# Performance work log

Hardware: AMD Instinct MI355X
Metric: run time of the kernel (lower is better)

## Reference

```python
import jax, jax.numpy as jnp
import numpy as np

N_NODES = 100000

def _norm_coeffs(edge_index, n_nodes):
    # PyG GCNConv default: add self-loops, symmetric normalization D^-1/2 A D^-1/2
    src = jnp.concatenate([edge_index[0], jnp.arange(n_nodes, dtype=edge_index.dtype)])
    dst = jnp.concatenate([edge_index[1], jnp.arange(n_nodes, dtype=edge_index.dtype)])
    deg = jax.ops.segment_sum(jnp.ones_like(dst, dtype=jnp.float32), dst, num_segments=n_nodes)
    dinv = jnp.where(deg > 0, jax.lax.rsqrt(deg), 0.0)
    norm = dinv[src] * dinv[dst]  # [E + N]
    return src, dst, norm

def _gcn_conv(x, W, b, src, dst, norm, n_nodes):
    h = x @ W                       # [N, out] dense transform first (PyG order)
    msg = h[src] * norm[:, None]    # gather + scale, [E+N, out]
    out = jax.ops.segment_sum(msg, dst, num_segments=n_nodes)  # scatter-add aggregate
    return out + b

def setup_inputs() -> dict:
    key = jax.random.key(0)
    ks = jax.random.split(key, 8)
    in_feats, h_feats, num_classes = 128, 128, 64
    n_edges = 1_600_000
    x = jax.random.normal(ks[0], (N_NODES, in_feats), dtype=jnp.float32)
    edge_index = jax.random.randint(ks[1], (2, n_edges), 0, N_NODES, dtype=jnp.int64)
    def glorot(k, fi, fo):
        s = jnp.sqrt(6.0 / (fi + fo))
        return jax.random.uniform(k, (fi, fo), jnp.float32, -s, s)
    return {
        "x": x,
        "edge_index": edge_index,
        "W0": glorot(ks[2], in_feats, h_feats), "b0": jnp.zeros((h_feats,), jnp.float32),
        "W1": glorot(ks[3], h_feats, h_feats), "b1": jnp.zeros((h_feats,), jnp.float32),
        "W2": glorot(ks[4], h_feats, num_classes), "b2": jnp.zeros((num_classes,), jnp.float32),
    }

def reference(x, edge_index, W0, b0, W1, b1, W2, b2):
    n_nodes = x.shape[0]
    src, dst, norm = _norm_coeffs(edge_index, n_nodes)
    # layer 0 + 1: ReLU between (dropout is identity in eval mode)
    h = jax.nn.relu(_gcn_conv(x, W0, b0, src, dst, norm, n_nodes))
    h = jax.nn.relu(_gcn_conv(h, W1, b1, src, dst, norm, n_nodes))
    # final layer: no activation
    return _gcn_conv(h, W2, b2, src, dst, norm, n_nodes)
```

## Files before the change

kernel.cpp:

```cpp
#include <hip/hip_runtime.h>
#include <hip/hip_bf16.h>
#include <stdint.h>


typedef __attribute__((ext_vector_type(8))) short bf16x8;
typedef __attribute__((ext_vector_type(4))) float f32x4;

__device__ __forceinline__ float bflo(uint32_t u) { return __uint_as_float(u << 16); }
__device__ __forceinline__ float bfhi(uint32_t u) { return __uint_as_float(u & 0xffff0000u); }
__device__ __forceinline__ unsigned short f2bf(float f) {
    uint32_t x = __float_as_uint(f);
    return (unsigned short)((x + 0x7fffu + ((x >> 16) & 1u)) >> 16);
}

__global__ __launch_bounds__(256) void k_deg_rank(const int* __restrict__ dst,
                                                  int* __restrict__ deg,
                                                  int* __restrict__ rank, int E) {
    int e = blockIdx.x * 256 + threadIdx.x;
    if (e < E) rank[e] = atomicAdd(&deg[dst[e]], 1);
}

__global__ __launch_bounds__(256) void k_dinv(const int* __restrict__ deg,
                                              float* __restrict__ dinv, int N) {
    int i = blockIdx.x * 256 + threadIdx.x;
    if (i < N) dinv[i] = rsqrtf((float)(deg[i] + 1));
}

__global__ __launch_bounds__(256) void k_scan_local(const int* __restrict__ deg,
                                                    int* __restrict__ incl,
                                                    int* __restrict__ bsum, int N) {
    __shared__ int part[256];
    int t = threadIdx.x;
    int idx0 = blockIdx.x * 1024 + t * 4;
    int4 lv = {0, 0, 0, 0};
    if (idx0 + 4 <= N) {
        lv = *(const int4*)&deg[idx0];
    } else {
        int* pv = (int*)&lv;
        for (int i = 0; i < 4; ++i) pv[i] = (idx0 + i < N) ? deg[idx0 + i] : 0;
    }
    int s = lv.x + lv.y + lv.z + lv.w;
    part[t] = s;
    __syncthreads();
    for (int off = 1; off < 256; off <<= 1) {
        int x = (t >= off) ? part[t - off] : 0;
        __syncthreads();
        part[t] += x;
        __syncthreads();
    }
    int run = (t == 0) ? 0 : part[t - 1];
    if (t == 255) bsum[blockIdx.x] = part[255];
    int4 ov;
    ov.x = run + lv.x;
    ov.y = ov.x + lv.y;
    ov.z = ov.y + lv.z;
    ov.w = ov.z + lv.w;
    if (idx0 + 4 <= N) {
        *(int4*)&incl[idx0] = ov;
    } else {
        int* po = (int*)&ov;
        for (int i = 0; i < 4; ++i)
            if (idx0 + i < N) incl[idx0 + i] = po[i];
    }
}

__global__ __launch_bounds__(256) void k_scan_tops(int* __restrict__ bsum, int nb,
                                                   int* __restrict__ row_ptr, int N) {
    __shared__ int part[256];
    int t = threadIdx.x;
    int v = (t < nb) ? bsum[t] : 0;
    part[t] = v;
    __syncthreads();
    for (int off = 1; off < 256; off <<= 1) {
        int x = (t >= off) ? part[t - off] : 0;
        __syncthreads();
        part[t] += x;
        __syncthreads();
    }
    if (t < nb) bsum[t] = part[t] - v;
    if (t == 255) row_ptr[N] = part[255];
}

__global__ __launch_bounds__(256) void k_scan_final(const int* __restrict__ incl,
                                                    const int* __restrict__ deg,
                                                    const int* __restrict__ bsum,
                                                    int* __restrict__ row_ptr, int N) {
    int i = blockIdx.x * 256 + threadIdx.x;
    if (i < N) row_ptr[i] = incl[i] - deg[i] + bsum[i >> 10];
}

__global__ __launch_bounds__(256) void k_scatter(const int* __restrict__ src,
                                                 const int* __restrict__ dst,
                                                 const int* __restrict__ rank,
                                                 const int* __restrict__ row_ptr,
                                                 int* __restrict__ col_idx, int E) {
    int e = blockIdx.x * 256 + threadIdx.x;
    if (e < E) {
        int d = dst[e];
        col_idx[row_ptr[d] + rank[e]] = src[e];
    }
}

__global__ __launch_bounds__(256) void k_prepw(const float* __restrict__ W0,
                                               const float* __restrict__ W1,
                                               const float* __restrict__ W2,
                                               unsigned short* __restrict__ wt0,
                                               unsigned short* __restrict__ wt1,
                                               unsigned short* __restrict__ wt2) {
    int id = blockIdx.x * 256 + threadIdx.x;
    const float* Wsrc;
    unsigned short* dst;
    int t, M, plane;
    if (id < 16384)      { t = id;         Wsrc = W0; dst = wt0; M = 128; plane = 16384; }
    else if (id < 32768) { t = id - 16384; Wsrc = W1; dst = wt1; M = 128; plane = 16384; }
    else if (id < 40960) { t = id - 32768; Wsrc = W2; dst = wt2; M = 64;  plane = 8192;  }
    else return;
    int k = (M == 128) ? (t >> 7) : (t >> 6);
    int c = (M == 128) ? (t & 127) : (t & 63);
    float v = Wsrc[k * M + c];
    unsigned short hi = f2bf(v);
    float lov = v - bflo((uint32_t)hi);
    dst[c * 128 + k]         = hi;
    dst[plane + c * 128 + k] = f2bf(lov);
}

template <int NCOL>
__global__ __launch_bounds__(256) void k_gemm_mfma(
    const float* __restrict__ A, const unsigned short* __restrict__ Wt,
    const float* __restrict__ dinv, unsigned short* __restrict__ H, int N) {
    constexpr int K = 128, KT = 64;
    constexpr int A_PLANE = 128 * KT;
    constexpr int W_PLANE = NCOL * KT;
    __shared__ __align__(16) unsigned short sm[2 * A_PLANE + 2 * W_PLANE];
    unsigned short* Ah  = sm;
    unsigned short* Al  = sm + A_PLANE;
    unsigned short* Whp = sm + 2 * A_PLANE;
    unsigned short* Wlp = sm + 2 * A_PLANE + W_PLANE;

    const int tid = threadIdx.x;
    const long r0 = (long)blockIdx.x * 128;
    const int w = tid >> 6, l = tid & 63;
    const int lr = l & 15, lk = l >> 4;
    constexpr int WR = (NCOL == 128) ? 4 : 2;
    const int wrow = (NCOL == 128) ? (w >> 1) * 64 : w * 32;
    const int wcol = (NCOL == 128) ? (w & 1) * 64 : 0;

    f32x4 acc[WR][4];
#pragma unroll
    for (int i = 0; i < WR; ++i)
#pragma unroll
        for (int j = 0; j < 4; ++j) acc[i][j] = (f32x4){0.f, 0.f, 0.f, 0.f};

    for (int kt = 0; kt < 2; ++kt) {
        if (kt) __syncthreads();
#pragma unroll
        for (int it = 0; it < 4; ++it) {
            int id = it * 256 + tid;
            int r = id >> 3, kc = id & 7;
            long gr = r0 + r;
            if (gr >= N) gr = N - 1;
            const float* ap = &A[gr * K + kt * KT + kc * 8];
            float4 v0 = *(const float4*)ap;
            float4 v1 = *(const float4*)(ap + 4);
            float vv[8] = {v0.x, v0.y, v0.z, v0.w, v1.x, v1.y, v1.z, v1.w};
            union { unsigned short u[8]; bf16x8 v; } ph, pl;
#pragma unroll
            for (int j = 0; j < 8; ++j) {
                unsigned short h = f2bf(vv[j]);
                ph.u[j] = h;
                pl.u[j] = f2bf(vv[j] - bflo((uint32_t)h));
            }
            int boff = r * 128 + ((kc * 16) ^ ((r & 7) << 4));
            *(bf16x8*)((char*)Ah + boff) = ph.v;
            *(bf16x8*)((char*)Al + boff) = pl.v;
        }
#pragma unroll
        for (int it = 0; it < NCOL / 32; ++it) {
            int id = it * 256 + tid;
            int c = id >> 3, kc = id & 7;
            const unsigned short* wp = &Wt[c * K + kt * KT + kc * 8];
            bf16x8 vh = *(const bf16x8*)wp;
            bf16x8 vl = *(const bf16x8*)(wp + NCOL * K);
            int boff = c * 128 + ((kc * 16) ^ ((c & 7) << 4));
            *(bf16x8*)((char*)Whp + boff) = vh;
            *(bf16x8*)((char*)Wlp + boff) = vl;
        }
        __syncthreads();
#pragma unroll
        for (int ks = 0; ks < 2; ++ks) {
            int kb = ks * 64 + lk * 16;
            bf16x8 bh[4], bl[4];
#pragma unroll
            for (int cf = 0; cf < 4; ++cf) {
                int c = wcol + cf * 16 + lr;
                int off = c * 128 + (kb ^ ((c & 7) << 4));
                bh[cf] = *(bf16x8*)((char*)Whp + off);
                bl[cf] = *(bf16x8*)((char*)Wlp + off);
            }
#pragma unroll
            for (int rf = 0; rf < WR; ++rf) {
                int r = wrow + rf * 16 + lr;
                int off = r * 128 + (kb ^ ((r & 7) << 4));
                bf16x8 ah = *(bf16x8*)((char*)Ah + off);
                bf16x8 al = *(bf16x8*)((char*)Al + off);
#pragma unroll
                for (int cf = 0; cf < 4; ++cf) {
                    acc[rf][cf] = __builtin_amdgcn_mfma_f32_16x16x32_bf16(ah, bh[cf], acc[rf][cf], 0, 0, 0);
                    acc[rf][cf] = __builtin_amdgcn_mfma_f32_16x16x32_bf16(al, bh[cf], acc[rf][cf], 0, 0, 0);
                    acc[rf][cf] = __builtin_amdgcn_mfma_f32_16x16x32_bf16(ah, bl[cf], acc[rf][cf], 0, 0, 0);
                }
            }
        }
    }
#pragma unroll
    for (int rf = 0; rf < WR; ++rf) {
        long rb = r0 + wrow + rf * 16 + lk * 4;
#pragma unroll
        for (int reg = 0; reg < 4; ++reg) {
            long r = rb + reg;
            if (r < N) {
                float dv = dinv[r];
#pragma unroll
                for (int cf = 0; cf < 4; ++cf) {
                    int c = wcol + cf * 16 + lr;
                    H[r * NCOL + c] = f2bf(dv * acc[rf][cf][reg]);
                }
            }
        }
    }
}

template <int F, bool RELU>
__global__ __launch_bounds__(256) void k_agg(const unsigned short* __restrict__ H,
                                             const int* __restrict__ row_ptr,
                                             const int* __restrict__ col_idx,
                                             const float* __restrict__ dinv,
                                             const float* __restrict__ bias,
                                             float* __restrict__ Y, int N) {
    int lane = threadIdx.x & 63;
    int node = blockIdx.x * 4 + (threadIdx.x >> 6);
    if (node >= N) return;

    float acc0, acc1 = 0.f;
    if constexpr (F == 128) {
        uint32_t u = *(const uint32_t*)&H[(size_t)node * 128 + lane * 2];
        acc0 = bflo(u);
        acc1 = bfhi(u);
    } else {
        acc0 = bflo((uint32_t)H[(size_t)node * F + lane]);
    }

    int start = row_ptr[node], end = row_ptr[node + 1];
    for (int base = start; base < end; base += 64) {
        int n = end - base;
        int sidx = 0;
        if (lane < n) sidx = col_idx[base + lane];
        int cnt = n < 64 ? n : 64;
        int j = 0;
        for (; j + 4 <= cnt; j += 4) {
            int s0 = __shfl(sidx, j),     s1 = __shfl(sidx, j + 1);
            int s2 = __shfl(sidx, j + 2), s3 = __shfl(sidx, j + 3);
            if constexpr (F == 128) {
                uint32_t u0 = *(const uint32_t*)&H[(size_t)s0 * 128 + lane * 2];
                uint32_t u1 = *(const uint32_t*)&H[(size_t)s1 * 128 + lane * 2];
                uint32_t u2 = *(const uint32_t*)&H[(size_t)s2 * 128 + lane * 2];
                uint32_t u3 = *(const uint32_t*)&H[(size_t)s3 * 128 + lane * 2];
                acc0 += bflo(u0); acc1 += bfhi(u0);
                acc0 += bflo(u1); acc1 += bfhi(u1);
                acc0 += bflo(u2); acc1 += bfhi(u2);
                acc0 += bflo(u3); acc1 += bfhi(u3);
            } else {
                acc0 += bflo((uint32_t)H[(size_t)s0 * F + lane]);
                acc0 += bflo((uint32_t)H[(size_t)s1 * F + lane]);
                acc0 += bflo((uint32_t)H[(size_t)s2 * F + lane]);
                acc0 += bflo((uint32_t)H[(size_t)s3 * F + lane]);
            }
        }
        for (; j < cnt; ++j) {
            int s = __shfl(sidx, j);
            if constexpr (F == 128) {
                uint32_t u = *(const uint32_t*)&H[(size_t)s * 128 + lane * 2];
                acc0 += bflo(u);
                acc1 += bfhi(u);
            } else {
                acc0 += bflo((uint32_t)H[(size_t)s * F + lane]);
            }
        }
    }

    float dv = dinv[node];
    if constexpr (F == 128) {
        float2 b = *(const float2*)&bias[lane * 2];
        float y0 = dv * acc0 + b.x, y1 = dv * acc1 + b.y;
        if (RELU) { y0 = fmaxf(y0, 0.f); y1 = fmaxf(y1, 0.f); }
        float2 o; o.x = y0; o.y = y1;
        *(float2*)&Y[(size_t)node * 128 + lane * 2] = o;
    } else {
        float y = dv * acc0 + bias[lane];
        if (RELU) y = fmaxf(y, 0.f);
        Y[(size_t)node * F + lane] = y;
    }
}

extern "C" void kernel_launch(void* const* d_in, const int* in_sizes, int n_in,
                              void* d_out, int out_size, void* d_ws, size_t ws_size,
                              hipStream_t stream) {
    const float* x  = (const float*)d_in[0];
    const int* eidx = (const int*)d_in[1];
    const float* W0 = (const float*)d_in[2];
    const float* b0 = (const float*)d_in[3];
    const float* W1 = (const float*)d_in[4];
    const float* b1 = (const float*)d_in[5];
    const float* W2 = (const float*)d_in[6];
    const float* b2 = (const float*)d_in[7];
    float* out = (float*)d_out;

    const int N = in_sizes[0] / 128;
    const int E = in_sizes[1] / 2;
    const int* srcp = eidx;
    const int* dstp = eidx + E;

    char* p = (char*)d_ws;
    auto take = [&](size_t bytes) {
        char* r = p;
        p += (bytes + 255) & ~(size_t)255;
        return r;
    };
    int*            deg     = (int*)take((size_t)N * 4);
    int*            rank    = (int*)take((size_t)E * 4);
    int*            row_ptr = (int*)take((size_t)(N + 1) * 4);
    float*          dinv    = (float*)take((size_t)N * 4);
    int*            col_idx = (int*)take((size_t)E * 4);
    unsigned short* hbuf    = (unsigned short*)take((size_t)N * 128 * 2);
    float*          ybuf    = (float*)take((size_t)N * 128 * 4);
    int*            incl    = (int*)take((size_t)N * 4);
    int*            bsum    = (int*)take((size_t)256 * 4);
    unsigned short* wt0     = (unsigned short*)take((size_t)2 * 16384 * 2);
    unsigned short* wt1     = (unsigned short*)take((size_t)2 * 16384 * 2);
    unsigned short* wt2     = (unsigned short*)take((size_t)2 * 8192 * 2);

    hipMemsetAsync(deg, 0, (size_t)N * 4, stream);

    k_deg_rank<<<(E + 255) / 256, 256, 0, stream>>>(dstp, deg, rank, E);
    k_dinv<<<(N + 255) / 256, 256, 0, stream>>>(deg, dinv, N);
    k_prepw<<<160, 256, 0, stream>>>(W0, W1, W2, wt0, wt1, wt2);

    int nb = (N + 1023) / 1024;
    k_scan_local<<<nb, 256, 0, stream>>>(deg, incl, bsum, N);
    k_scan_tops<<<1, 256, 0, stream>>>(bsum, nb, row_ptr, N);
    k_scan_final<<<(N + 255) / 256, 256, 0, stream>>>(incl, deg, bsum, row_ptr, N);

    k_scatter<<<(E + 255) / 256, 256, 0, stream>>>(srcp, dstp, rank, row_ptr,
                                                   col_idx, E);

    int gemm_grid = (N + 127) / 128;
    int agg_grid  = (N + 3) / 4;

    k_gemm_mfma<128><<<gemm_grid, 256, 0, stream>>>(x, wt0, dinv, hbuf, N);
    k_agg<128, true><<<agg_grid, 256, 0, stream>>>(hbuf, row_ptr, col_idx,
                                                   dinv, b0, ybuf, N);
    k_gemm_mfma<128><<<gemm_grid, 256, 0, stream>>>(ybuf, wt1, dinv, hbuf, N);
    k_agg<128, true><<<agg_grid, 256, 0, stream>>>(hbuf, row_ptr, col_idx,
                                                   dinv, b1, ybuf, N);
    k_gemm_mfma<64><<<gemm_grid, 256, 0, stream>>>(ybuf, wt2, dinv, hbuf, N);
    k_agg<64, false><<<agg_grid, 256, 0, stream>>>(hbuf, row_ptr, col_idx,
                                                   dinv, b2, out, N);
}
```

Measured before the change: 457.3 us.

## Privatize degree-count atomics per XCC to cut cross-die contention

The degree histogram and rank atomics are split into eight per-XCC count arrays, indexed by the hardware XCC id, so atomics from different dies hit different cache lines. A merge kernel turns the per-XCC counts into exclusive offsets and computes the total degree and dinv. The scatter then adds the XCC offset to the local rank. This costs an 8x larger memset and counter buffer plus an extra read in the scatter, in exchange for more local atomics.

Result: no change. 462.6 us (+1.2%).

```diff
diff --git a/kernel.cpp b/kernel.cpp
--- a/kernel.cpp
+++ b/kernel.cpp
@@ -13,17 +13,38 @@
     return (unsigned short)((x + 0x7fffu + ((x >> 16) & 1u)) >> 16);
 }
 
+__device__ __forceinline__ int xcc_id() {
+    int x;
+    asm volatile("s_getreg_b32 %0, hwreg(HW_REG_XCC_ID)" : "=s"(x));
+    return x & 7;
+}
+
 __global__ __launch_bounds__(256) void k_deg_rank(const int* __restrict__ dst,
-                                                  int* __restrict__ deg,
-                                                  int* __restrict__ rank, int E) {
+                                                  int* __restrict__ scnt,
+                                                  int* __restrict__ rank,
+                                                  int N, int E) {
     int e = blockIdx.x * 256 + threadIdx.x;
-    if (e < E) rank[e] = atomicAdd(&deg[dst[e]], 1);
-}
-
-__global__ __launch_bounds__(256) void k_dinv(const int* __restrict__ deg,
-                                              float* __restrict__ dinv, int N) {
+    int xc = xcc_id();
+    if (e < E) {
+        int r = atomicAdd(&scnt[xc * N + dst[e]], 1);
+        rank[e] = (xc << 28) | r;
+    }
+}
+
+__global__ __launch_bounds__(256) void k_merge(int* __restrict__ scnt,
+                                               int* __restrict__ deg,
+                                               float* __restrict__ dinv, int N) {
     int i = blockIdx.x * 256 + threadIdx.x;
-    if (i < N) dinv[i] = rsqrtf((float)(deg[i] + 1));
+    if (i >= N) return;
+    int sum = 0;
+#pragma unroll
+    for (int s = 0; s < 8; ++s) {
+        int c = scnt[s * N + i];
+        scnt[s * N + i] = sum;
+        sum += c;
+    }
+    deg[i] = sum;
+    dinv[i] = rsqrtf((float)(sum + 1));
 }
 
 __global__ __launch_bounds__(256) void k_scan_local(const int* __restrict__ deg,
@@ -93,11 +114,15 @@
                                                  const int* __restrict__ dst,
                                                  const int* __restrict__ rank,
                                                  const int* __restrict__ row_ptr,
-                                                 int* __restrict__ col_idx, int E) {
+                                                 const int* __restrict__ scnt,
+                                                 int* __restrict__ col_idx,
+                                                 int N, int E) {
     int e = blockIdx.x * 256 + threadIdx.x;
     if (e < E) {
         int d = dst[e];
-        col_idx[row_ptr[d] + rank[e]] = src[e];
+        int pr = rank[e];
+        int s = pr >> 28, lr = pr & 0x0fffffff;
+        col_idx[row_ptr[d] + scnt[s * N + d] + lr] = src[e];
     }
 }
 
@@ -326,6 +351,7 @@
         p += (bytes + 255) & ~(size_t)255;
         return r;
     };
+    int*            scnt    = (int*)take((size_t)8 * N * 4);
     int*            deg     = (int*)take((size_t)N * 4);
     int*            rank    = (int*)take((size_t)E * 4);
     int*            row_ptr = (int*)take((size_t)(N + 1) * 4);
@@ -339,10 +365,10 @@
     unsigned short* wt1     = (unsigned short*)take((size_t)2 * 16384 * 2);
     unsigned short* wt2     = (unsigned short*)take((size_t)2 * 8192 * 2);
 
-    hipMemsetAsync(deg, 0, (size_t)N * 4, stream);
-
-    k_deg_rank<<<(E + 255) / 256, 256, 0, stream>>>(dstp, deg, rank, E);
-    k_dinv<<<(N + 255) / 256, 256, 0, stream>>>(deg, dinv, N);
+    hipMemsetAsync(scnt, 0, (size_t)8 * N * 4, stream);
+
+    k_deg_rank<<<(E + 255) / 256, 256, 0, stream>>>(dstp, scnt, rank, N, E);
+    k_merge<<<(N + 255) / 256, 256, 0, stream>>>(scnt, deg, dinv, N);
     k_prepw<<<160, 256, 0, stream>>>(W0, W1, W2, wt0, wt1, wt2);
 
     int nb = (N + 1023) / 1024;
@@ -351,7 +377,7 @@
     k_scan_final<<<(N + 255) / 256, 256, 0, stream>>>(incl, deg, bsum, row_ptr, N);
 
     k_scatter<<<(E + 255) / 256, 256, 0, stream>>>(srcp, dstp, rank, row_ptr,
-                                                   col_idx, E);
+                                                   scnt, col_idx, N, E);
 
     int gemm_grid = (N + 127) / 128;
     int agg_grid  = (N + 3) / 4;
```
